# Optimization experiments

Measured on AMD Instinct MI355X. Metric: run time of the kernel, lower is better.

Reference implementation:

```python
import jax, jax.numpy as jnp
import numpy as np

EPS = float(np.finfo(np.float32).eps)
H = 256          # hidden_size
K = 10           # num_event_types
B, S = 32, 4096  # batch, seq_len


def _linear_params(kw, kb, fan_in, fan_out):
    # torch nn.Linear default init (uniform +-1/sqrt(fan_in)), then abs + clamp(min=eps)
    bound = 1.0 / np.sqrt(fan_in)
    w = jnp.clip(jnp.abs(jax.random.uniform(kw, (fan_out, fan_in), minval=-bound, maxval=bound, dtype=jnp.float32)), EPS)
    b = jnp.clip(jnp.abs(jax.random.uniform(kb, (fan_out,), minval=-bound, maxval=bound, dtype=jnp.float32)), EPS)
    return w, b


def setup_inputs() -> dict:
    key = jax.random.key(0)
    ks = jax.random.split(key, 12)
    w1, b1 = _linear_params(ks[0], ks[1], 1, H)        # layer_dense_1
    w2, b2 = _linear_params(ks[2], ks[3], 2 * H, H)    # layer_dense_2
    wA, bA = _linear_params(ks[4], ks[5], H, H)        # module_list[0]
    wB, bB = _linear_params(ks[6], ks[7], H, H)        # module_list[1]
    w3, b3 = _linear_params(ks[8], ks[9], H, K)        # layer_dense_3 linear
    hidden_states = jax.random.normal(ks[10], (B, S, H), dtype=jnp.float32)
    time_delta_seqs = jax.random.uniform(ks[11], (B, S), dtype=jnp.float32)
    return dict(hidden_states=hidden_states, time_delta_seqs=time_delta_seqs,
                w1=w1, b1=b1, w2=w2, b2=b2, wA=wA, bA=bA, wB=wB, bB=bB, w3=w3, b3=b3)


def _cumul_hazard(td, h, w1, b1, w2, b2, wA, bA, wB, bB, w3, b3):
    # layer_dense_1: Linear(1 -> H) on td[..., None]
    t = td[..., None] * w1[:, 0] + b1                      # [B,S,H]
    out = jnp.tanh(jnp.concatenate([h, t], axis=-1) @ w2.T + b2)  # [B,S,H]
    out = jnp.tanh(out @ wA.T + bA)
    out = jnp.tanh(out @ wB.T + bB)
    return jax.nn.softplus(out @ w3.T + b3)                # [B,S,K]


def reference(hidden_states, time_delta_seqs, w1, b1, w2, b2, wA, bA, wB, bB, w3, b3):
    f = lambda td: _cumul_hazard(td, hidden_states, w1, b1, w2, b2, wA, bA, wB, bB, w3, b3)
    # Each output element depends only on its own t[b,s] (elementwise in time),
    # so a single forward-mode JVP with tangent=ones yields the exact per-element
    # derivative for ALL event types at once (fuses torch's per-type grad loop).
    integral_lambda, d_dt = jax.jvp(f, (time_delta_seqs,), (jnp.ones_like(time_delta_seqs),))
    # torch takes grad of .mean() over [B,S], which scales the derivative by 1/(B*S)
    derivative_integral_lambda = d_dt / time_delta_seqs.size
    return integral_lambda, derivative_integral_lambda
```

## Files before the change

### kernel.cpp

```cpp
#include <hip/hip_runtime.h>
#include <hip/hip_bf16.h>
#include <stdint.h>

typedef __bf16 bf16x8 __attribute__((ext_vector_type(8)));
typedef __bf16 bf16x4 __attribute__((ext_vector_type(4)));
typedef float  f32x4  __attribute__((ext_vector_type(4)));
typedef float  f32x2  __attribute__((ext_vector_type(2)));

#define MFMA16(a,b,c) __builtin_amdgcn_mfma_f32_16x16x32_bf16((a),(b),(c),0,0,0)

static constexpr int H_   = 256;
static constexpr int KEV  = 10;
static constexpr int NTOK = 32 * 4096;

__device__ __forceinline__ float ptanh(float x){
    float t = x * x;
    float n = fmaf(t, t + 105.0f, 945.0f);
    float d = fmaf(t, fmaf(t, 15.0f, 420.0f), 945.0f);
    float r = x * n * __builtin_amdgcn_rcpf(d);
    return fminf(1.0f, fmaxf(-1.0f, r));
}

__device__ __forceinline__ bf16x8 cvtFrag(const float* p){
    f32x4 a = *(const f32x4*)p;
    f32x4 b = *(const f32x4*)(p + 4);
    bf16x8 r;
    #pragma unroll
    for (int j = 0; j < 4; ++j){ r[j] = (__bf16)a[j]; r[4 + j] = (__bf16)b[j]; }
    return r;
}

__global__ void prep_vc(const float* __restrict__ w1, const float* __restrict__ b1,
                        const float* __restrict__ w2, const float* __restrict__ b2,
                        float* __restrict__ vc){
    int j = blockIdx.x * 4 + (threadIdx.x >> 6);
    int l = threadIdx.x & 63;
    const float* row = w2 + (size_t)j * (2 * H_) + H_;
    float v = 0.f, cc = 0.f;
    #pragma unroll
    for (int i = 0; i < 4; ++i){
        int k = l + 64 * i;
        float w = row[k];
        v  += w * w1[k];
        cc += w * b1[k];
    }
    #pragma unroll
    for (int off = 32; off; off >>= 1){
        v  += __shfl_down(v,  off, 64);
        cc += __shfl_down(cc, off, 64);
    }
    if (l == 0){ vc[j] = v; vc[H_ + j] = cc + b2[j]; }
}

__global__ void prep_pack(const float* __restrict__ w2, const float* __restrict__ wA,
                          const float* __restrict__ wB, __hip_bfloat16* __restrict__ pk){
    int b  = blockIdx.x;
    int L  = b >> 4, n0 = b & 15;
    const float* W = (L == 0) ? w2 : ((L == 1) ? wA : wB);
    int K = (L == 0) ? 2 * H_ : H_;
    __hip_bfloat16* dst = pk + (size_t)b * 4096;
    int t = threadIdx.x;
    #pragma unroll
    for (int u = 0; u < 2; ++u){
        int slot = t * 2 + u;
        int s = slot >> 6, q = (slot >> 4) & 3, c = slot & 15;
        const float* src = W + (size_t)(n0 * 16 + c) * K + 32 * s + 8 * q;
        #pragma unroll
        for (int j = 0; j < 8; ++j) dst[slot * 8 + j] = __float2bfloat16(src[j]);
    }
}

__global__ __launch_bounds__(256, 1) void chfn_kernel(
    const float* __restrict__ hs, const float* __restrict__ td,
    const __hip_bfloat16* __restrict__ wpk,
    const float* __restrict__ bA, const float* __restrict__ bB,
    const float* __restrict__ w3, const float* __restrict__ b3,
    const float* __restrict__ vc,
    float* __restrict__ out)
{
    extern __shared__ __hip_bfloat16 smem[];
    __hip_bfloat16* sA = smem;
    __hip_bfloat16* sD = smem + 128 * H_;

    const int tid  = threadIdx.x;
    const int wave = tid >> 6;
    const int lane = tid & 63;
    const int q    = lane >> 4;
    const int c    = lane & 15;
    const int tb   = blockIdx.x * 128 + wave * 32;
    const int baseRow = wave * 32;

    const bf16x8* wp = (const bf16x8*)wpk;
    const int ws = q * 16 + c;

    bf16x8 W0[8], W1[8];
    {
        const bf16x8* b = wp + ws;
        #pragma unroll
        for (int s = 0; s < 8; ++s) W0[s] = b[s * 64];
    }

    bf16x8 aF0[8], aF1[8], aB0[8], aB1[8];
    {
        const float* h0 = hs + (size_t)(tb + c) * H_ + 8 * q;
        const float* h1 = hs + (size_t)(tb + 16 + c) * H_ + 8 * q;
        #pragma unroll
        for (int s = 0; s < 8; ++s){
            aF0[s] = cvtFrag(h0 + 32 * s);
            aF1[s] = cvtFrag(h1 + 32 * s);
        }
    }
    float td0 = td[tb + c];
    float td1 = td[tb + 16 + c];

    #pragma unroll 2
    for (int n0 = 0; n0 < 16; ++n0){
        bf16x8* cur = (n0 & 1) ? W1 : W0;
        bf16x8* nxt = (n0 & 1) ? W0 : W1;
        {
            const bf16x8* b = wp + (size_t)(n0 + 1) * 512 + ws;
            #pragma unroll
            for (int s = 0; s < 8; ++s) nxt[s] = b[s * 64];
        }
        f32x4 v4 = *(const f32x4*)(vc + n0 * 16 + 4 * q);
        f32x4 c4 = *(const f32x4*)(vc + H_ + n0 * 16 + 4 * q);
        f32x4 fa0 = {0.f,0.f,0.f,0.f}, fb0 = {0.f,0.f,0.f,0.f};
        f32x4 fa1 = {0.f,0.f,0.f,0.f}, fb1 = {0.f,0.f,0.f,0.f};
        #pragma unroll
        for (int s = 0; s < 4; ++s){
            fa0 = MFMA16(cur[s],     aF0[s],     fa0);
            fa1 = MFMA16(cur[s],     aF1[s],     fa1);
            fb0 = MFMA16(cur[s + 4], aF0[s + 4], fb0);
            fb1 = MFMA16(cur[s + 4], aF1[s + 4], fb1);
        }
        #pragma unroll
        for (int t = 0; t < 2; ++t){
            const f32x4& fa = t ? fa1 : fa0;
            const f32x4& fb = t ? fb1 : fb0;
            float tdg = t ? td1 : td0;
            bf16x4 pa, pd;
            #pragma unroll
            for (int r = 0; r < 4; ++r){
                float x  = (fa[r] + fb[r]) + fmaf(tdg, v4[r], c4[r]);
                float th = ptanh(x);
                float dd = fmaf(-th, th, 1.0f) * v4[r];
                pa[r] = (__bf16)th; pd[r] = (__bf16)dd;
            }
            int off = (baseRow + 16 * t + c) * H_ +
                      (((2 * n0 + (q >> 1) + c) & 31) << 3) + ((q & 1) << 2);
            *(bf16x4*)((void*)(sA + off)) = pa;
            *(bf16x4*)((void*)(sD + off)) = pd;
        }
    }

    #pragma unroll 1
    for (int L = 0; L < 2; ++L){
        const float* bias = L ? bB : bA;
        {
            const __hip_bfloat16* a0 = sA + (baseRow + c) * H_;
            const __hip_bfloat16* a1 = sA + (baseRow + 16 + c) * H_;
            const __hip_bfloat16* d0 = sD + (baseRow + c) * H_;
            const __hip_bfloat16* d1 = sD + (baseRow + 16 + c) * H_;
            #pragma unroll
            for (int s = 0; s < 8; ++s){
                int chn = (((4 * s + q) + c) & 31) << 3;
                aF0[s] = *(const bf16x8*)(a0 + chn);
                aF1[s] = *(const bf16x8*)(a1 + chn);
                aB0[s] = *(const bf16x8*)(d0 + chn);
                aB1[s] = *(const bf16x8*)(d1 + chn);
            }
        }
        #pragma unroll 2
        for (int n0 = 0; n0 < 16; ++n0){
            int g = 16 * (L + 1) + n0;
            bf16x8* cur = (n0 & 1) ? W1 : W0;
            bf16x8* nxt = (n0 & 1) ? W0 : W1;
            {
                int gn = g + 1; if (gn > 47) gn = 47;
                const bf16x8* b = wp + (size_t)gn * 512 + ws;
                #pragma unroll
                for (int s = 0; s < 8; ++s) nxt[s] = b[s * 64];
            }
            f32x4 b4 = *(const f32x4*)(bias + n0 * 16 + 4 * q);
            f32x4 fa0 = {0.f,0.f,0.f,0.f}, fb0 = {0.f,0.f,0.f,0.f};
            f32x4 ga0 = {0.f,0.f,0.f,0.f}, gb0 = {0.f,0.f,0.f,0.f};
            f32x4 fa1 = {0.f,0.f,0.f,0.f}, fb1 = {0.f,0.f,0.f,0.f};
            f32x4 ga1 = {0.f,0.f,0.f,0.f}, gb1 = {0.f,0.f,0.f,0.f};
            #pragma unroll
            for (int s = 0; s < 4; ++s){
                fa0 = MFMA16(cur[s],     aF0[s],     fa0);
                ga0 = MFMA16(cur[s],     aB0[s],     ga0);
                fa1 = MFMA16(cur[s],     aF1[s],     fa1);
                ga1 = MFMA16(cur[s],     aB1[s],     ga1);
                fb0 = MFMA16(cur[s + 4], aF0[s + 4], fb0);
                gb0 = MFMA16(cur[s + 4], aB0[s + 4], gb0);
                fb1 = MFMA16(cur[s + 4], aF1[s + 4], fb1);
                gb1 = MFMA16(cur[s + 4], aB1[s + 4], gb1);
            }
            #pragma unroll
            for (int t = 0; t < 2; ++t){
                const f32x4& fa = t ? fa1 : fa0;  const f32x4& fb = t ? fb1 : fb0;
                const f32x4& ga = t ? ga1 : ga0;  const f32x4& gb = t ? gb1 : gb0;
                bf16x4 pa, pd;
                #pragma unroll
                for (int r = 0; r < 4; ++r){
                    float th = ptanh((fa[r] + fb[r]) + b4[r]);
                    float dd = fmaf(-th, th, 1.0f) * (ga[r] + gb[r]);
                    pa[r] = (__bf16)th; pd[r] = (__bf16)dd;
                }
                int off = (baseRow + 16 * t + c) * H_ +
                          (((2 * n0 + (q >> 1) + c) & 31) << 3) + ((q & 1) << 2);
                *(bf16x4*)((void*)(sA + off)) = pa;
                *(bf16x4*)((void*)(sD + off)) = pd;
            }
        }
    }

    {
        const __hip_bfloat16* a0 = sA + (baseRow + c) * H_;
        const __hip_bfloat16* a1 = sA + (baseRow + 16 + c) * H_;
        const __hip_bfloat16* d0 = sD + (baseRow + c) * H_;
        const __hip_bfloat16* d1 = sD + (baseRow + 16 + c) * H_;
        #pragma unroll
        for (int s = 0; s < 8; ++s){
            int chn = (((4 * s + q) + c) & 31) << 3;
            aF0[s] = *(const bf16x8*)(a0 + chn);
            aF1[s] = *(const bf16x8*)(a1 + chn);
            aB0[s] = *(const bf16x8*)(d0 + chn);
            aB1[s] = *(const bf16x8*)(d1 + chn);
        }
        int crow = (c < KEV) ? c : 0;
        const float* wp3 = w3 + (size_t)crow * H_ + 8 * q;
        bf16x8 w3f[8];
        #pragma unroll
        for (int s = 0; s < 8; ++s) w3f[s] = cvtFrag(wp3 + 32 * s);

        f32x4 fa0 = {0.f,0.f,0.f,0.f}, fb0 = {0.f,0.f,0.f,0.f};
        f32x4 ga0 = {0.f,0.f,0.f,0.f}, gb0 = {0.f,0.f,0.f,0.f};
        f32x4 fa1 = {0.f,0.f,0.f,0.f}, fb1 = {0.f,0.f,0.f,0.f};
        f32x4 ga1 = {0.f,0.f,0.f,0.f}, gb1 = {0.f,0.f,0.f,0.f};
        #pragma unroll
        for (int s = 0; s < 4; ++s){
            fa0 = MFMA16(w3f[s],     aF0[s],     fa0);
            ga0 = MFMA16(w3f[s],     aB0[s],     ga0);
            fa1 = MFMA16(w3f[s],     aF1[s],     fa1);
            ga1 = MFMA16(w3f[s],     aB1[s],     ga1);
            fb0 = MFMA16(w3f[s + 4], aF0[s + 4], fb0);
            gb0 = MFMA16(w3f[s + 4], aB0[s + 4], gb0);
            fb1 = MFMA16(w3f[s + 4], aF1[s + 4], fb1);
            gb1 = MFMA16(w3f[s + 4], aB1[s + 4], gb1);
        }
        int fbase = 4 * q;
        #pragma unroll
        for (int t = 0; t < 2; ++t){
            const f32x4& fa = t ? fa1 : fa0;  const f32x4& fb = t ? fb1 : fb0;
            const f32x4& ga = t ? ga1 : ga0;  const f32x4& gb = t ? gb1 : gb0;
            size_t token = tb + 16 * t + c;
            float sp[4], dv[4];
            #pragma unroll
            for (int r = 0; r < 4; ++r){
                int fi   = fbase + r;
                float bn = b3[(fi < KEV) ? fi : (KEV - 1)];
                float z  = (fa[r] + fb[r]) + bn;
                float a  = fabsf(z);
                float e  = __builtin_amdgcn_exp2f(-1.4426950408889634f * a);
                sp[r] = fmaxf(z, 0.f) + 0.69314718055994531f * __builtin_amdgcn_logf(1.0f + e);
                float sg = __builtin_amdgcn_rcpf(1.0f + e);
                sg = (z >= 0.f) ? sg : 1.0f - sg;
                dv[r] = sg * (ga[r] + gb[r]) * (1.0f / 131072.0f);
            }
            float* o0 = out + token * KEV + fbase;
            float* o1 = out + (size_t)NTOK * KEV + token * KEV + fbase;
            if (q < 2){
                *(f32x2*)o0       = (f32x2){sp[0], sp[1]};
                *(f32x2*)(o0 + 2) = (f32x2){sp[2], sp[3]};
                *(f32x2*)o1       = (f32x2){dv[0], dv[1]};
                *(f32x2*)(o1 + 2) = (f32x2){dv[2], dv[3]};
            } else if (q == 2){
                *(f32x2*)o0 = (f32x2){sp[0], sp[1]};
                *(f32x2*)o1 = (f32x2){dv[0], dv[1]};
            }
        }
    }
}

extern "C" void kernel_launch(void* const* d_in, const int* in_sizes, int n_in,
                              void* d_out, int out_size, void* d_ws, size_t ws_size,
                              hipStream_t stream){
    const float* hs = (const float*)d_in[0];
    const float* td = (const float*)d_in[1];
    const float* w1 = (const float*)d_in[2];
    const float* b1 = (const float*)d_in[3];
    const float* w2 = (const float*)d_in[4];
    const float* b2 = (const float*)d_in[5];
    const float* wA = (const float*)d_in[6];
    const float* bA = (const float*)d_in[7];
    const float* wB = (const float*)d_in[8];
    const float* bB = (const float*)d_in[9];
    const float* w3 = (const float*)d_in[10];
    const float* b3 = (const float*)d_in[11];

    float*          vc  = (float*)d_ws;
    __hip_bfloat16* wpk = (__hip_bfloat16*)((char*)d_ws + 4096);
    float*          outp = (float*)d_out;

    (void)hipFuncSetAttribute((const void*)chfn_kernel,
                              hipFuncAttributeMaxDynamicSharedMemorySize, 131072);

    prep_vc  <<<64, 256, 0, stream>>>(w1, b1, w2, b2, vc);
    prep_pack<<<48, 256, 0, stream>>>(w2, wA, wB, wpk);
    chfn_kernel<<<NTOK / 128, 256, 131072, stream>>>(hs, td, wpk, bA, bB, w3, b3, vc, outp);
}
```

Baseline: 353.2 us.

## Halve tokens per wave to cut registers and LDS, allowing two blocks per CU

```diff
diff --git a/kernel.cpp b/kernel.cpp
--- a/kernel.cpp
+++ b/kernel.cpp
@@ -70,7 +70,7 @@
     }
 }
 
-__global__ __launch_bounds__(256, 1) void chfn_kernel(
+__global__ __launch_bounds__(256, 2) void chfn_kernel(
     const float* __restrict__ hs, const float* __restrict__ td,
     const __hip_bfloat16* __restrict__ wpk,
     const float* __restrict__ bA, const float* __restrict__ bB,
@@ -78,17 +78,16 @@
     const float* __restrict__ vc,
     float* __restrict__ out)
 {
-    extern __shared__ __hip_bfloat16 smem[];
-    __hip_bfloat16* sA = smem;
-    __hip_bfloat16* sD = smem + 128 * H_;
+    __shared__ __hip_bfloat16 sA[4 * 16 * H_];
+    __shared__ __hip_bfloat16 sD[4 * 16 * H_];
 
     const int tid  = threadIdx.x;
     const int wave = tid >> 6;
     const int lane = tid & 63;
     const int q    = lane >> 4;
     const int c    = lane & 15;
-    const int tb   = blockIdx.x * 128 + wave * 32;
-    const int baseRow = wave * 32;
+    const int tb   = blockIdx.x * 64 + wave * 16;
+    const int wrow = wave * 16;
 
     const bf16x8* wp = (const bf16x8*)wpk;
     const int ws = q * 16 + c;
@@ -100,18 +99,13 @@
         for (int s = 0; s < 8; ++s) W0[s] = b[s * 64];
     }
 
-    bf16x8 aF0[8], aF1[8], aB0[8], aB1[8];
+    bf16x8 aF[8], aB[8];
     {
         const float* h0 = hs + (size_t)(tb + c) * H_ + 8 * q;
-        const float* h1 = hs + (size_t)(tb + 16 + c) * H_ + 8 * q;
-        #pragma unroll
-        for (int s = 0; s < 8; ++s){
-            aF0[s] = cvtFrag(h0 + 32 * s);
-            aF1[s] = cvtFrag(h1 + 32 * s);
-        }
-    }
-    float td0 = td[tb + c];
-    float td1 = td[tb + 16 + c];
+        #pragma unroll
+        for (int s = 0; s < 8; ++s) aF[s] = cvtFrag(h0 + 32 * s);
+    }
+    float myTd = td[tb + c];
 
     #pragma unroll 2
     for (int n0 = 0; n0 < 16; ++n0){
@@ -124,50 +118,37 @@
         }
         f32x4 v4 = *(const f32x4*)(vc + n0 * 16 + 4 * q);
         f32x4 c4 = *(const f32x4*)(vc + H_ + n0 * 16 + 4 * q);
-        f32x4 fa0 = {0.f,0.f,0.f,0.f}, fb0 = {0.f,0.f,0.f,0.f};
-        f32x4 fa1 = {0.f,0.f,0.f,0.f}, fb1 = {0.f,0.f,0.f,0.f};
+        f32x4 fa = c4;
+        f32x4 fb = {0.f,0.f,0.f,0.f};
         #pragma unroll
         for (int s = 0; s < 4; ++s){
-            fa0 = MFMA16(cur[s],     aF0[s],     fa0);
-            fa1 = MFMA16(cur[s],     aF1[s],     fa1);
-            fb0 = MFMA16(cur[s + 4], aF0[s + 4], fb0);
-            fb1 = MFMA16(cur[s + 4], aF1[s + 4], fb1);
-        }
-        #pragma unroll
-        for (int t = 0; t < 2; ++t){
-            const f32x4& fa = t ? fa1 : fa0;
-            const f32x4& fb = t ? fb1 : fb0;
-            float tdg = t ? td1 : td0;
-            bf16x4 pa, pd;
-            #pragma unroll
-            for (int r = 0; r < 4; ++r){
-                float x  = (fa[r] + fb[r]) + fmaf(tdg, v4[r], c4[r]);
-                float th = ptanh(x);
-                float dd = fmaf(-th, th, 1.0f) * v4[r];
-                pa[r] = (__bf16)th; pd[r] = (__bf16)dd;
-            }
-            int off = (baseRow + 16 * t + c) * H_ +
-                      (((2 * n0 + (q >> 1) + c) & 31) << 3) + ((q & 1) << 2);
-            *(bf16x4*)((void*)(sA + off)) = pa;
-            *(bf16x4*)((void*)(sD + off)) = pd;
-        }
+            fa = MFMA16(cur[s],     aF[s],     fa);
+            fb = MFMA16(cur[s + 4], aF[s + 4], fb);
+        }
+        bf16x4 pa, pd;
+        #pragma unroll
+        for (int r = 0; r < 4; ++r){
+            float x  = fmaf(myTd, v4[r], fa[r] + fb[r]);
+            float th = ptanh(x);
+            float dd = fmaf(-th, th, 1.0f) * v4[r];
+            pa[r] = (__bf16)th; pd[r] = (__bf16)dd;
+        }
+        int off = (wrow + c) * H_ + (((2 * n0 + (q >> 1) + c) & 31) << 3) + ((q & 1) << 2);
+        *(bf16x4*)((void*)(sA + off)) = pa;
+        *(bf16x4*)((void*)(sD + off)) = pd;
     }
 
     #pragma unroll 1
     for (int L = 0; L < 2; ++L){
         const float* bias = L ? bB : bA;
         {
-            const __hip_bfloat16* a0 = sA + (baseRow + c) * H_;
-            const __hip_bfloat16* a1 = sA + (baseRow + 16 + c) * H_;
-            const __hip_bfloat16* d0 = sD + (baseRow + c) * H_;
-            const __hip_bfloat16* d1 = sD + (baseRow + 16 + c) * H_;
+            const __hip_bfloat16* a0 = sA + (wrow + c) * H_;
+            const __hip_bfloat16* d0 = sD + (wrow + c) * H_;
             #pragma unroll
             for (int s = 0; s < 8; ++s){
                 int chn = (((4 * s + q) + c) & 31) << 3;
-                aF0[s] = *(const bf16x8*)(a0 + chn);
-                aF1[s] = *(const bf16x8*)(a1 + chn);
-                aB0[s] = *(const bf16x8*)(d0 + chn);
-                aB1[s] = *(const bf16x8*)(d1 + chn);
+                aF[s] = *(const bf16x8*)(a0 + chn);
+                aB[s] = *(const bf16x8*)(d0 + chn);
             }
         }
         #pragma unroll 2
@@ -182,104 +163,77 @@
                 for (int s = 0; s < 8; ++s) nxt[s] = b[s * 64];
             }
             f32x4 b4 = *(const f32x4*)(bias + n0 * 16 + 4 * q);
-            f32x4 fa0 = {0.f,0.f,0.f,0.f}, fb0 = {0.f,0.f,0.f,0.f};
-            f32x4 ga0 = {0.f,0.f,0.f,0.f}, gb0 = {0.f,0.f,0.f,0.f};
-            f32x4 fa1 = {0.f,0.f,0.f,0.f}, fb1 = {0.f,0.f,0.f,0.f};
-            f32x4 ga1 = {0.f,0.f,0.f,0.f}, gb1 = {0.f,0.f,0.f,0.f};
+            f32x4 fa = b4;
+            f32x4 fb = {0.f,0.f,0.f,0.f};
+            f32x4 ga = {0.f,0.f,0.f,0.f};
+            f32x4 gb = {0.f,0.f,0.f,0.f};
             #pragma unroll
             for (int s = 0; s < 4; ++s){
-                fa0 = MFMA16(cur[s],     aF0[s],     fa0);
-                ga0 = MFMA16(cur[s],     aB0[s],     ga0);
-                fa1 = MFMA16(cur[s],     aF1[s],     fa1);
-                ga1 = MFMA16(cur[s],     aB1[s],     ga1);
-                fb0 = MFMA16(cur[s + 4], aF0[s + 4], fb0);
-                gb0 = MFMA16(cur[s + 4], aB0[s + 4], gb0);
-                fb1 = MFMA16(cur[s + 4], aF1[s + 4], fb1);
-                gb1 = MFMA16(cur[s + 4], aB1[s + 4], gb1);
-            }
-            #pragma unroll
-            for (int t = 0; t < 2; ++t){
-                const f32x4& fa = t ? fa1 : fa0;  const f32x4& fb = t ? fb1 : fb0;
-                const f32x4& ga = t ? ga1 : ga0;  const f32x4& gb = t ? gb1 : gb0;
-                bf16x4 pa, pd;
-                #pragma unroll
-                for (int r = 0; r < 4; ++r){
-                    float th = ptanh((fa[r] + fb[r]) + b4[r]);
-                    float dd = fmaf(-th, th, 1.0f) * (ga[r] + gb[r]);
-                    pa[r] = (__bf16)th; pd[r] = (__bf16)dd;
-                }
-                int off = (baseRow + 16 * t + c) * H_ +
-                          (((2 * n0 + (q >> 1) + c) & 31) << 3) + ((q & 1) << 2);
-                *(bf16x4*)((void*)(sA + off)) = pa;
-                *(bf16x4*)((void*)(sD + off)) = pd;
-            }
+                fa = MFMA16(cur[s],     aF[s],     fa);
+                ga = MFMA16(cur[s],     aB[s],     ga);
+                fb = MFMA16(cur[s + 4], aF[s + 4], fb);
+                gb = MFMA16(cur[s + 4], aB[s + 4], gb);
+            }
+            bf16x4 pa, pd;
+            #pragma unroll
+            for (int r = 0; r < 4; ++r){
+                float th = ptanh(fa[r] + fb[r]);
+                float dd = fmaf(-th, th, 1.0f) * (ga[r] + gb[r]);
+                pa[r] = (__bf16)th; pd[r] = (__bf16)dd;
+            }
+            int off = (wrow + c) * H_ + (((2 * n0 + (q >> 1) + c) & 31) << 3) + ((q & 1) << 2);
+            *(bf16x4*)((void*)(sA + off)) = pa;
+            *(bf16x4*)((void*)(sD + off)) = pd;
         }
     }
 
     {
-        const __hip_bfloat16* a0 = sA + (baseRow + c) * H_;
-        const __hip_bfloat16* a1 = sA + (baseRow + 16 + c) * H_;
-        const __hip_bfloat16* d0 = sD + (baseRow + c) * H_;
-        const __hip_bfloat16* d1 = sD + (baseRow + 16 + c) * H_;
+        const __hip_bfloat16* a0 = sA + (wrow + c) * H_;
+        const __hip_bfloat16* d0 = sD + (wrow + c) * H_;
         #pragma unroll
         for (int s = 0; s < 8; ++s){
             int chn = (((4 * s + q) + c) & 31) << 3;
-            aF0[s] = *(const bf16x8*)(a0 + chn);
-            aF1[s] = *(const bf16x8*)(a1 + chn);
-            aB0[s] = *(const bf16x8*)(d0 + chn);
-            aB1[s] = *(const bf16x8*)(d1 + chn);
+            aF[s] = *(const bf16x8*)(a0 + chn);
+            aB[s] = *(const bf16x8*)(d0 + chn);
         }
         int crow = (c < KEV) ? c : 0;
         const float* wp3 = w3 + (size_t)crow * H_ + 8 * q;
-        bf16x8 w3f[8];
-        #pragma unroll
-        for (int s = 0; s < 8; ++s) w3f[s] = cvtFrag(wp3 + 32 * s);
-
-        f32x4 fa0 = {0.f,0.f,0.f,0.f}, fb0 = {0.f,0.f,0.f,0.f};
-        f32x4 ga0 = {0.f,0.f,0.f,0.f}, gb0 = {0.f,0.f,0.f,0.f};
-        f32x4 fa1 = {0.f,0.f,0.f,0.f}, fb1 = {0.f,0.f,0.f,0.f};
-        f32x4 ga1 = {0.f,0.f,0.f,0.f}, gb1 = {0.f,0.f,0.f,0.f};
+        f32x4 fa = {0.f,0.f,0.f,0.f}, fb = {0.f,0.f,0.f,0.f};
+        f32x4 ga = {0.f,0.f,0.f,0.f}, gb = {0.f,0.f,0.f,0.f};
         #pragma unroll
         for (int s = 0; s < 4; ++s){
-            fa0 = MFMA16(w3f[s],     aF0[s],     fa0);
-            ga0 = MFMA16(w3f[s],     aB0[s],     ga0);
-            fa1 = MFMA16(w3f[s],     aF1[s],     fa1);
-            ga1 = MFMA16(w3f[s],     aB1[s],     ga1);
-            fb0 = MFMA16(w3f[s + 4], aF0[s + 4], fb0);
-            gb0 = MFMA16(w3f[s + 4], aB0[s + 4], gb0);
-            fb1 = MFMA16(w3f[s + 4], aF1[s + 4], fb1);
-            gb1 = MFMA16(w3f[s + 4], aB1[s + 4], gb1);
+            bf16x8 bv0 = cvtFrag(wp3 + 32 * s);
+            bf16x8 bv1 = cvtFrag(wp3 + 32 * (s + 4));
+            fa = MFMA16(bv0, aF[s],     fa);
+            ga = MFMA16(bv0, aB[s],     ga);
+            fb = MFMA16(bv1, aF[s + 4], fb);
+            gb = MFMA16(bv1, aB[s + 4], gb);
         }
         int fbase = 4 * q;
-        #pragma unroll
-        for (int t = 0; t < 2; ++t){
-            const f32x4& fa = t ? fa1 : fa0;  const f32x4& fb = t ? fb1 : fb0;
-            const f32x4& ga = t ? ga1 : ga0;  const f32x4& gb = t ? gb1 : gb0;
-            size_t token = tb + 16 * t + c;
-            float sp[4], dv[4];
-            #pragma unroll
-            for (int r = 0; r < 4; ++r){
-                int fi   = fbase + r;
-                float bn = b3[(fi < KEV) ? fi : (KEV - 1)];
-                float z  = (fa[r] + fb[r]) + bn;
-                float a  = fabsf(z);
-                float e  = __builtin_amdgcn_exp2f(-1.4426950408889634f * a);
-                sp[r] = fmaxf(z, 0.f) + 0.69314718055994531f * __builtin_amdgcn_logf(1.0f + e);
-                float sg = __builtin_amdgcn_rcpf(1.0f + e);
-                sg = (z >= 0.f) ? sg : 1.0f - sg;
-                dv[r] = sg * (ga[r] + gb[r]) * (1.0f / 131072.0f);
-            }
-            float* o0 = out + token * KEV + fbase;
-            float* o1 = out + (size_t)NTOK * KEV + token * KEV + fbase;
-            if (q < 2){
-                *(f32x2*)o0       = (f32x2){sp[0], sp[1]};
-                *(f32x2*)(o0 + 2) = (f32x2){sp[2], sp[3]};
-                *(f32x2*)o1       = (f32x2){dv[0], dv[1]};
-                *(f32x2*)(o1 + 2) = (f32x2){dv[2], dv[3]};
-            } else if (q == 2){
-                *(f32x2*)o0 = (f32x2){sp[0], sp[1]};
-                *(f32x2*)o1 = (f32x2){dv[0], dv[1]};
-            }
+        size_t token = tb + c;
+        float sp[4], dv[4];
+        #pragma unroll
+        for (int r = 0; r < 4; ++r){
+            int fi   = fbase + r;
+            float bn = b3[(fi < KEV) ? fi : (KEV - 1)];
+            float z  = (fa[r] + fb[r]) + bn;
+            float a  = fabsf(z);
+            float e  = __builtin_amdgcn_exp2f(-1.4426950408889634f * a);
+            sp[r] = fmaxf(z, 0.f) + 0.69314718055994531f * __builtin_amdgcn_logf(1.0f + e);
+            float sg = __builtin_amdgcn_rcpf(1.0f + e);
+            sg = (z >= 0.f) ? sg : 1.0f - sg;
+            dv[r] = sg * (ga[r] + gb[r]) * (1.0f / 131072.0f);
+        }
+        float* o0 = out + token * KEV + fbase;
+        float* o1 = out + (size_t)NTOK * KEV + token * KEV + fbase;
+        if (q < 2){
+            *(f32x2*)o0       = (f32x2){sp[0], sp[1]};
+            *(f32x2*)(o0 + 2) = (f32x2){sp[2], sp[3]};
+            *(f32x2*)o1       = (f32x2){dv[0], dv[1]};
+            *(f32x2*)(o1 + 2) = (f32x2){dv[2], dv[3]};
+        } else if (q == 2){
+            *(f32x2*)o0 = (f32x2){sp[0], sp[1]};
+            *(f32x2*)o1 = (f32x2){dv[0], dv[1]};
         }
     }
 }
@@ -304,10 +258,7 @@
     __hip_bfloat16* wpk = (__hip_bfloat16*)((char*)d_ws + 4096);
     float*          outp = (float*)d_out;
 
-    (void)hipFuncSetAttribute((const void*)chfn_kernel,
-                              hipFuncAttributeMaxDynamicSharedMemorySize, 131072);
-
     prep_vc  <<<64, 256, 0, stream>>>(w1, b1, w2, b2, vc);
     prep_pack<<<48, 256, 0, stream>>>(w2, wA, wB, wpk);
-    chfn_kernel<<<NTOK / 128, 256, 131072, stream>>>(hs, td, wpk, bA, bB, w3, b3, vc, outp);
-}
+    chfn_kernel<<<NTOK / 64, 256, 0, stream>>>(hs, td, wpk, bA, bB, w3, b3, vc, outp);
+}
```

Result: faster. 330.6 us (-6.4%).
